# Performance work log

Hardware: AMD Instinct MI355X
Metric: run time of the kernel (lower is better)

The kernel has to match this reference:

```python
import jax, jax.numpy as jnp
import numpy as np

EPS = 1e-5

def layernorm(x, w, b):
    m = jnp.mean(x, axis=-1, keepdims=True)
    v = jnp.var(x, axis=-1, keepdims=True)
    return (x - m) * jax.lax.rsqrt(v + EPS) * w + b

def setup_inputs() -> dict:
    key = jax.random.key(0)
    ks = jax.random.split(key, 20)
    B, N, D, H, C = 4, 2048, 512, 8, 3
    HID = int(D * 4.0 * (2.0 / 3.0))  # SwiGLU hidden = 1365
    g = lambda k, shape, s: (jax.random.normal(k, shape, jnp.float32) * s)
    return {
        "x": g(ks[0], (B, N, D), 1.0),
        "coords": jax.random.uniform(ks[1], (B, N, C), jnp.float32),
        "ln1_w": jnp.ones((D,), jnp.float32),
        "ln1_b": jnp.zeros((D,), jnp.float32),
        "ln2_w": jnp.ones((D,), jnp.float32),
        "ln2_b": jnp.zeros((D,), jnp.float32),
        "Wqkv": g(ks[2], (D, 3 * D), D ** -0.5),
        "bqkv": jnp.zeros((3 * D,), jnp.float32),
        "Wo": g(ks[3], (D, D), D ** -0.5),
        "bo": jnp.zeros((D,), jnp.float32),
        "Wc": g(ks[4], (C, H), 0.1),
        "bc": jnp.zeros((H,), jnp.float32),
        "W1": g(ks[5], (D, HID), D ** -0.5),
        "b1": jnp.zeros((HID,), jnp.float32),
        "W2": g(ks[6], (D, HID), D ** -0.5),
        "b2": jnp.zeros((HID,), jnp.float32),
        "W3": g(ks[7], (HID, D), HID ** -0.5),
        "b3": jnp.zeros((D,), jnp.float32),
    }

def reference(x, coords, ln1_w, ln1_b, ln2_w, ln2_b, Wqkv, bqkv, Wo, bo,
              Wc, bc, W1, b1, W2, b2, W3, b3):
    B, N, D = x.shape
    H = bc.shape[0]
    dh = D // H
    # --- coord-aware patch attention (pre-norm) ---
    h = layernorm(x, ln1_w, ln1_b)
    qkv = h @ Wqkv + bqkv                                # [B,N,3D]
    q, k, v = jnp.split(qkv, 3, axis=-1)
    to_heads = lambda t: t.reshape(B, N, H, dh).transpose(0, 2, 1, 3)  # [B,H,N,dh]
    q, k, v = to_heads(q), to_heads(k), to_heads(v)
    scores = jnp.einsum("bhnd,bhmd->bhnm", q, k) / np.sqrt(dh)
    rel = coords[:, :, None, :] - coords[:, None, :, :]  # [B,N,N,C]
    bias = jnp.einsum("bnmc,ch->bhnm", rel, Wc) + bc[None, :, None, None]
    attn = jax.nn.softmax(scores + bias, axis=-1)
    o = jnp.einsum("bhnm,bhmd->bhnd", attn, v)
    o = o.transpose(0, 2, 1, 3).reshape(B, N, D)
    x = x + (o @ Wo + bo)                                # residual 1
    # --- SwiGLU FFN (pre-norm) ---
    h2 = layernorm(x, ln2_w, ln2_b)
    ff = jax.nn.silu(h2 @ W1 + b1) * (h2 @ W2 + b2)
    x = x + (ff @ W3 + b3)                               # residual 2
    return x
```

## Files before the change

### kernel.cpp

```cpp
#include <hip/hip_runtime.h>
#include <hip/hip_bf16.h>
#include <math.h>

#define B_   4
#define N_   2048
#define D_   512
#define H_   8
#define DH_  64
#define C_   3
#define HID_ 1365
#define HIDP 1408
#define ROWS_ (B_*N_)
#define TD_  (3*D_)

typedef __attribute__((ext_vector_type(8))) short short8;
typedef __attribute__((ext_vector_type(4))) float floatx4;

#define MFMA16(a,b,c) __builtin_amdgcn_mfma_f32_16x16x32_bf16(a,b,c,0,0,0)

typedef __attribute__((address_space(3))) unsigned lds_u32;
typedef __attribute__((address_space(1))) unsigned glb_u32;

__device__ __forceinline__ short sh(float v){
  union { __hip_bfloat16 b; short s; } u;
  u.b = __float2bfloat16(v);
  return u.s;
}

__device__ __forceinline__ int swz(int col, int row){
  return (col & ~63) | (col & 7) | ((((col >> 3) & 7) ^ (row & 7)) << 3);
}

template<int ROWS, int PITCH>
__device__ __forceinline__ void stageG(short* __restrict__ lds,
    const short* __restrict__ g, int ldg, int t){
  const int LPR = PITCH/8;
  const int RPI = 64/LPR;
  const int PW  = (ROWS/RPI)/4;
  int lane = t & 63, w = t >> 6;
  #pragma unroll
  for (int i = 0; i < PW; ++i){
    int r0  = (w*PW + i)*RPI;
    int row = r0 + lane/LPR;
    const short* ga = g + (size_t)row*ldg + (lane % LPR)*8;
    short* la = lds + r0*PITCH;
    __builtin_amdgcn_global_load_lds((const glb_u32*)ga, (lds_u32*)la, 16, 0, 0);
  }
}

__device__ __forceinline__ short8 fragS(const short* __restrict__ lds, int pitch,
    int mbase, int lane, int kk){
  int row  = mbase + (lane & 15);
  int seg  = (kk >> 3) + (lane >> 4);
  int phys = seg ^ (row & 7);
  return *(const short8*)(lds + row*pitch + phys*8);
}

__device__ __forceinline__ short8 fragP(const short* __restrict__ lds,
    int mbase, int lane, int kk){
  return *(const short8*)(lds + (mbase + (lane & 15))*136 + kk + ((lane >> 4) << 3));
}

__global__ __launch_bounds__(256) void convT_all(
    const float* __restrict__ Wqkv, const float* __restrict__ Wo,
    const float* __restrict__ W1, const float* __restrict__ W2,
    const float* __restrict__ W3,
    short* __restrict__ Wtqkv, short* __restrict__ Wto,
    short* __restrict__ Wt1, short* __restrict__ Wt2, short* __restrict__ Wt3,
    const float* __restrict__ coords, const float* __restrict__ Wc,
    float* __restrict__ tv,
    const float* __restrict__ x, const float* __restrict__ ln1_w,
    const float* __restrict__ ln1_b, short* __restrict__ h){
  int id = blockIdx.x;
  int t = threadIdx.x;
  if (id >= 3392){
    int row = id - 3392;
    size_t base = (size_t)row * D_;
    float v0 = x[base + t];
    float v1 = x[base + t + 256];
    float s  = v0 + v1;
    float s2 = v0*v0 + v1*v1;
    #pragma unroll
    for (int off = 32; off >= 1; off >>= 1){
      s  += __shfl_xor(s,  off, 64);
      s2 += __shfl_xor(s2, off, 64);
    }
    __shared__ float red[8];
    int lane = t & 63, wv = t >> 6;
    if (lane == 0){ red[wv] = s; red[4+wv] = s2; }
    __syncthreads();
    float sum  = red[0]+red[1]+red[2]+red[3];
    float sum2 = red[4]+red[5]+red[6]+red[7];
    float mean = sum * (1.0f/D_);
    float var  = sum2 * (1.0f/D_) - mean*mean;
    float inv  = rsqrtf(fmaxf(var, 0.f) + 1e-5f);
    h[base + swz(t,     row)] = sh((v0-mean)*inv*ln1_w[t]     + ln1_b[t]);
    h[base + swz(t+256, row)] = sh((v1-mean)*inv*ln1_w[t+256] + ln1_b[t+256]);
    return;
  }
  if (id >= 3136){
    int idx = (id - 3136)*256 + t;
    int n = idx & (N_-1);
    int hh = (idx >> 11) & (H_-1);
    int b = idx >> 14;
    float s = 0.f;
    #pragma unroll
    for (int cc = 0; cc < C_; ++cc)
      s += coords[((size_t)(b*N_+n))*C_ + cc] * Wc[cc*H_ + hh];
    tv[idx] = s;
    return;
  }
  __shared__ float tile[32][33];
  const float* in; short* out; int K, NN, Kp, nx;
  if (id < 768)      { in=Wqkv; out=Wtqkv; K=512;  NN=1536; Kp=512;  nx=48; }
  else if (id < 1024){ in=Wo;   out=Wto;   K=512;  NN=512;  Kp=512;  nx=16; id-=768; }
  else if (id < 1728){ in=W1;   out=Wt1;   K=512;  NN=HID_; Kp=512;  nx=44; id-=1024; }
  else if (id < 2432){ in=W2;   out=Wt2;   K=512;  NN=HID_; Kp=512;  nx=44; id-=1728; }
  else               { in=W3;   out=Wt3;   K=HID_; NN=512;  Kp=HIDP; nx=16; id-=2432; }
  int nt0 = (id % nx)*32, kt0 = (id / nx)*32;
  int r = t >> 5, cc = t & 31;
  #pragma unroll
  for (int i=0;i<4;++i){
    int k = kt0 + i*8 + r, n = nt0 + cc;
    tile[i*8+r][cc] = (k<K && n<NN) ? in[(size_t)k*NN + n] : 0.f;
  }
  __syncthreads();
  #pragma unroll
  for (int i=0;i<4;++i){
    int n = nt0 + i*8 + r, k = kt0 + cc;
    out[(size_t)n*Kp + swz(k, n)] = sh(tile[cc][i*8+r]);
  }
}

__global__ __launch_bounds__(256) void ln_kernel(const float* __restrict__ x,
        const float* __restrict__ w, const float* __restrict__ b,
        short* __restrict__ out){
  int row = blockIdx.x;
  size_t base = (size_t)row * D_;
  int t = threadIdx.x;
  float v0 = x[base + t];
  float v1 = x[base + t + 256];
  float s  = v0 + v1;
  float s2 = v0*v0 + v1*v1;
  #pragma unroll
  for (int off = 32; off >= 1; off >>= 1){
    s  += __shfl_xor(s,  off, 64);
    s2 += __shfl_xor(s2, off, 64);
  }
  __shared__ float red[8];
  int lane = t & 63, wv = t >> 6;
  if (lane == 0){ red[wv] = s; red[4+wv] = s2; }
  __syncthreads();
  float sum  = red[0]+red[1]+red[2]+red[3];
  float sum2 = red[4]+red[5]+red[6]+red[7];
  float mean = sum * (1.0f/D_);
  float var  = sum2 * (1.0f/D_) - mean*mean;
  float inv  = rsqrtf(fmaxf(var, 0.f) + 1e-5f);
  out[base + swz(t,     row)] = sh((v0-mean)*inv*w[t]     + b[t]);
  out[base + swz(t+256, row)] = sh((v1-mean)*inv*w[t+256] + b[t+256]);
}

__global__ __launch_bounds__(256) void qkv_gemm(
    const short* __restrict__ A, const short* __restrict__ Bt,
    const float* __restrict__ bias,
    short* __restrict__ qb, short* __restrict__ kb, short* __restrict__ vbt){
  __shared__ short As[128*64];
  __shared__ short Bs[128*64];
  int t = threadIdx.x;
  int lane = t & 63, w = t >> 6;
  int wr = (w >> 1) * 64, wc = (w & 1) * 64;
  int col0 = blockIdx.x * 128, row0 = blockIdx.y * 128;
  floatx4 acc[4][4];
  #pragma unroll
  for (int mt=0;mt<4;++mt)
    #pragma unroll
    for (int nt=0;nt<4;++nt) acc[mt][nt] = (floatx4){0.f,0.f,0.f,0.f};
  for (int k0 = 0; k0 < D_; k0 += 64){
    __syncthreads();
    stageG<128,64>(As, A  + (size_t)row0*D_ + k0, D_, t);
    stageG<128,64>(Bs, Bt + (size_t)col0*D_ + k0, D_, t);
    __syncthreads();
    #pragma unroll
    for (int kk = 0; kk < 64; kk += 32){
      short8 af[4], bf[4];
      #pragma unroll
      for (int mt=0;mt<4;++mt) af[mt] = fragS(As, 64, wr+mt*16, lane, kk);
      #pragma unroll
      for (int nt=0;nt<4;++nt) bf[nt] = fragS(Bs, 64, wc+nt*16, lane, kk);
      #pragma unroll
      for (int mt=0;mt<4;++mt)
        #pragma unroll
        for (int nt=0;nt<4;++nt)
          acc[mt][nt] = MFMA16(af[mt], bf[nt], acc[mt][nt]);
    }
  }
  int quad = lane >> 4, c = lane & 15;
  #pragma unroll
  for (int mt=0;mt<4;++mt){
    #pragma unroll
    for (int nt=0;nt<4;++nt){
      #pragma unroll
      for (int r=0;r<4;++r){
        int row = row0 + wr + mt*16 + quad*4 + r;
        int col = col0 + wc + nt*16 + c;
        float v = acc[mt][nt][r] + bias[col];
        int bidx = row >> 11, n = row & (N_-1);
        int which = col >> 9, d = col & (D_-1), hh = d >> 6, hd = d & 63;
        short sv = sh(v);
        if (which == 0)
          qb[(((size_t)(bidx*H_ + hh))*N_ + n)*DH_ + swz(hd, n)] = sv;
        else if (which == 1)
          kb[(((size_t)(bidx*H_ + hh))*N_ + n)*DH_ + swz(hd, n)] = sv;
        else
          vbt[(((size_t)(bidx*H_ + hh))*DH_ + hd)*N_ + swz(n, hd)] = sv;
      }
    }
  }
}

__global__ __launch_bounds__(256) void gemm64(
    const short* __restrict__ A, int lda,
    const short* __restrict__ Bt, int Ktot,
    const float* __restrict__ bias,
    const float* __restrict__ resid, float* __restrict__ outF){
  __shared__ short As[128*64];
  __shared__ short Bs[64*64];
  int t = threadIdx.x, lane = t & 63, w = t >> 6;
  int wr = w * 32;
  int col0 = blockIdx.x * 64, row0 = blockIdx.y * 128;
  floatx4 acc[2][4];
  #pragma unroll
  for (int mt=0;mt<2;++mt)
    #pragma unroll
    for (int nt=0;nt<4;++nt) acc[mt][nt] = (floatx4){0.f,0.f,0.f,0.f};
  for (int k0 = 0; k0 < Ktot; k0 += 64){
    __syncthreads();
    stageG<128,64>(As, A  + (size_t)row0*lda + k0, lda, t);
    stageG<64,64> (Bs, Bt + (size_t)col0*Ktot + k0, Ktot, t);
    __syncthreads();
    #pragma unroll
    for (int kk = 0; kk < 64; kk += 32){
      short8 af[2], bf[4];
      #pragma unroll
      for (int mt=0;mt<2;++mt) af[mt] = fragS(As, 64, wr+mt*16, lane, kk);
      #pragma unroll
      for (int nt=0;nt<4;++nt) bf[nt] = fragS(Bs, 64, nt*16, lane, kk);
      #pragma unroll
      for (int mt=0;mt<2;++mt)
        #pragma unroll
        for (int nt=0;nt<4;++nt)
          acc[mt][nt] = MFMA16(af[mt], bf[nt], acc[mt][nt]);
    }
  }
  int quad = lane >> 4, c = lane & 15;
  #pragma unroll
  for (int mt=0;mt<2;++mt){
    #pragma unroll
    for (int nt=0;nt<4;++nt){
      #pragma unroll
      for (int r=0;r<4;++r){
        int row = row0 + wr + mt*16 + quad*4 + r;
        int col = col0 + nt*16 + c;
        size_t idx = (size_t)row*D_ + col;
        outF[idx] = acc[mt][nt][r] + bias[col] + resid[idx];
      }
    }
  }
}

__global__ __launch_bounds__(256) void gate_gemm(
    const short* __restrict__ A,
    const short* __restrict__ Bt1, const short* __restrict__ Bt2,
    const float* __restrict__ b1, const float* __restrict__ b2,
    short* __restrict__ ff){
  __shared__ short As[128*64];
  __shared__ short B1s[64*64];
  __shared__ short B2s[64*64];
  int t = threadIdx.x, lane = t & 63, w = t >> 6;
  int wr = (w >> 1) * 64, wc = (w & 1) * 32;
  int col0 = blockIdx.x * 64, row0 = blockIdx.y * 128;
  floatx4 a1[4][2], a2[4][2];
  #pragma unroll
  for (int mt=0;mt<4;++mt)
    #pragma unroll
    for (int nt=0;nt<2;++nt){
      a1[mt][nt] = (floatx4){0.f,0.f,0.f,0.f};
      a2[mt][nt] = (floatx4){0.f,0.f,0.f,0.f};
    }
  for (int k0 = 0; k0 < D_; k0 += 64){
    __syncthreads();
    stageG<128,64>(As, A + (size_t)row0*D_ + k0, D_, t);
    stageG<64,64>(B1s, Bt1 + (size_t)col0*D_ + k0, D_, t);
    stageG<64,64>(B2s, Bt2 + (size_t)col0*D_ + k0, D_, t);
    __syncthreads();
    #pragma unroll
    for (int kk = 0; kk < 64; kk += 32){
      short8 af[4], f1[2], f2[2];
      #pragma unroll
      for (int mt=0;mt<4;++mt) af[mt] = fragS(As, 64, wr+mt*16, lane, kk);
      #pragma unroll
      for (int nt=0;nt<2;++nt){
        f1[nt] = fragS(B1s, 64, wc+nt*16, lane, kk);
        f2[nt] = fragS(B2s, 64, wc+nt*16, lane, kk);
      }
      #pragma unroll
      for (int mt=0;mt<4;++mt)
        #pragma unroll
        for (int nt=0;nt<2;++nt){
          a1[mt][nt] = MFMA16(af[mt], f1[nt], a1[mt][nt]);
          a2[mt][nt] = MFMA16(af[mt], f2[nt], a2[mt][nt]);
        }
    }
  }
  int quad = lane >> 4, c = lane & 15;
  #pragma unroll
  for (int mt=0;mt<4;++mt){
    #pragma unroll
    for (int nt=0;nt<2;++nt){
      #pragma unroll
      for (int r=0;r<4;++r){
        int row = row0 + wr + mt*16 + quad*4 + r;
        int col = col0 + wc + nt*16 + c;
        float g1 = a1[mt][nt][r] + (col < HID_ ? b1[col] : 0.f);
        float g2 = a2[mt][nt][r] + (col < HID_ ? b2[col] : 0.f);
        float sig = 1.f / (1.f + __expf(-g1));
        ff[(size_t)row*HIDP + swz(col, row)] = sh(g1*sig*g2);
      }
    }
  }
}

__global__ __launch_bounds__(256) void attn_mfma(
    const short* __restrict__ qb, const short* __restrict__ kb,
    const short* __restrict__ vbt, const float* __restrict__ tv,
    short* __restrict__ o){
  __shared__ short Ks[128*64];
  __shared__ short Vt[64*128];
  __shared__ short Ps[128*136];
  __shared__ float tsh[128];
  int qt = blockIdx.x, h = blockIdx.y, b = blockIdx.z;
  int bh = b*H_ + h;
  int t = threadIdx.x, lane = t & 63, w = t >> 6;
  int quad = lane >> 4, c = lane & 15;
  stageG<128,64>(Ps, qb + ((size_t)bh*N_ + qt*128)*DH_, DH_, t);
  __syncthreads();
  short8 qf[2][2];
  #pragma unroll
  for (int mt=0;mt<2;++mt)
    #pragma unroll
    for (int kh=0;kh<2;++kh)
      qf[mt][kh] = fragS(Ps, 64, w*32 + mt*16, lane, kh*32);

  floatx4 O[2][4];
  float l_i[2][4];
  #pragma unroll
  for (int mt=0;mt<2;++mt){
    #pragma unroll
    for (int nt=0;nt<4;++nt) O[mt][nt] = (floatx4){0.f,0.f,0.f,0.f};
    #pragma unroll
    for (int r=0;r<4;++r) l_i[mt][r] = 0.f;
  }
  const short* Kbase = kb  + (size_t)bh*N_*DH_;
  const short* Vbase = vbt + (size_t)bh*DH_*N_;

  for (int kt = 0; kt < N_/128; ++kt){
    __syncthreads();
    stageG<128,64>(Ks, Kbase + (size_t)kt*128*DH_, DH_, t);
    stageG<64,128>(Vt, Vbase + kt*128, N_, t);
    if (t < 128) tsh[t] = tv[(size_t)bh*N_ + kt*128 + t];
    __syncthreads();

    floatx4 S[2][8];
    #pragma unroll
    for (int mt=0;mt<2;++mt)
      #pragma unroll
      for (int nt=0;nt<8;++nt) S[mt][nt] = (floatx4){0.f,0.f,0.f,0.f};
    #pragma unroll
    for (int kh=0;kh<2;++kh){
      short8 kf[8];
      #pragma unroll
      for (int nt=0;nt<8;++nt) kf[nt] = fragS(Ks, 64, nt*16, lane, kh*32);
      #pragma unroll
      for (int mt=0;mt<2;++mt)
        #pragma unroll
        for (int nt=0;nt<8;++nt)
          S[mt][nt] = MFMA16(qf[mt][kh], kf[nt], S[mt][nt]);
    }
    float ts[8];
    #pragma unroll
    for (int nt=0;nt<8;++nt) ts[nt] = tsh[nt*16 + c];
    #pragma unroll
    for (int mt=0;mt<2;++mt)
      #pragma unroll
      for (int r=0;r<4;++r){
        #pragma unroll
        for (int nt=0;nt<8;++nt){
          float p = __expf(S[mt][nt][r]*0.125f - ts[nt]);
          l_i[mt][r] += p;
          Ps[(w*32 + mt*16 + quad*4 + r)*136 + nt*16 + c] = sh(p);
        }
      }
    asm volatile("s_waitcnt lgkmcnt(0)" ::: "memory");
    #pragma unroll
    for (int kh=0;kh<4;++kh){
      short8 vf[4], pf[2];
      #pragma unroll
      for (int nt=0;nt<4;++nt) vf[nt] = fragS(Vt, 128, nt*16, lane, kh*32);
      #pragma unroll
      for (int mt=0;mt<2;++mt) pf[mt] = fragP(Ps, w*32 + mt*16, lane, kh*32);
      #pragma unroll
      for (int mt=0;mt<2;++mt)
        #pragma unroll
        for (int nt=0;nt<4;++nt)
          O[mt][nt] = MFMA16(pf[mt], vf[nt], O[mt][nt]);
    }
  }
  #pragma unroll
  for (int mt=0;mt<2;++mt){
    #pragma unroll
    for (int r=0;r<4;++r){
      float l = l_i[mt][r];
      #pragma unroll
      for (int off=1; off<16; off<<=1) l += __shfl_xor(l, off, 64);
      float invl = 1.f / l;
      int row = qt*128 + w*32 + mt*16 + quad*4 + r;
      #pragma unroll
      for (int nt=0;nt<4;++nt){
        int col = h*DH_ + nt*16 + c;
        o[((size_t)(b*N_ + row))*D_ + swz(col, row)] = sh(O[mt][nt][r]*invl);
      }
    }
  }
}

extern "C" void kernel_launch(void* const* d_in, const int* in_sizes, int n_in,
                              void* d_out, int out_size, void* d_ws, size_t ws_size,
                              hipStream_t stream){
  const float* x      = (const float*)d_in[0];
  const float* coords = (const float*)d_in[1];
  const float* ln1_w  = (const float*)d_in[2];
  const float* ln1_b  = (const float*)d_in[3];
  const float* ln2_w  = (const float*)d_in[4];
  const float* ln2_b  = (const float*)d_in[5];
  const float* Wqkv   = (const float*)d_in[6];
  const float* bqkv   = (const float*)d_in[7];
  const float* Wo     = (const float*)d_in[8];
  const float* bo     = (const float*)d_in[9];
  const float* Wc     = (const float*)d_in[10];
  const float* W1     = (const float*)d_in[12];
  const float* b1     = (const float*)d_in[13];
  const float* W2     = (const float*)d_in[14];
  const float* b2     = (const float*)d_in[15];
  const float* W3     = (const float*)d_in[16];
  const float* b3     = (const float*)d_in[17];

  char* ws = (char*)d_ws;
  short* Wtqkv = (short*)(ws);
  short* Wto   = (short*)(ws + 1572864);
  short* Wt1   = (short*)(ws + 2097152);
  short* Wt2   = (short*)(ws + 3538944);
  short* Wt3   = (short*)(ws + 4980736);
  float* tv    = (float*)(ws + 6422528);
  short* h     = (short*)(ws + 6684672);
  short* qb    = (short*)(ws + 15073280);
  short* kb    = (short*)(ws + 23461888);
  short* vbt   = (short*)(ws + 31850496);
  short* o     = h;
  short* h2    = h;
  short* ff    = qb;
  float* x1    = (float*)d_out;

  convT_all<<<dim3(11584), dim3(256), 0, stream>>>(Wqkv, Wo, W1, W2, W3,
      Wtqkv, Wto, Wt1, Wt2, Wt3, coords, Wc, tv, x, ln1_w, ln1_b, h);
  qkv_gemm<<<dim3(12,64), dim3(256), 0, stream>>>(h, Wtqkv, bqkv, qb, kb, vbt);
  attn_mfma<<<dim3(16,8,4), dim3(256), 0, stream>>>(qb, kb, vbt, tv, o);
  gemm64<<<dim3(8,64), dim3(256), 0, stream>>>(o, 512, Wto, 512, bo, x, x1);
  ln_kernel<<<dim3(ROWS_), dim3(256), 0, stream>>>(x1, ln2_w, ln2_b, h2);
  gate_gemm<<<dim3(22,64), dim3(256), 0, stream>>>(h2, Wt1, Wt2, b1, b2, ff);
  gemm64<<<dim3(8,64), dim3(256), 0, stream>>>(ff, HIDP, Wt3, HIDP, b3, x1, x1);
}
```

Baseline: 313.1 us.

## Double-buffer K/V in attention and keep P in registers via permlane swaps

Rewrites the attention kernel to double-buffer K and V tiles in LDS so the next tile loads while the current one computes, with one barrier per iteration instead of two. It computes S transposed (K as the A operand) so the probabilities can be packed into bf16 and rearranged with permlane32/16 swaps straight into PV MFMA operands, dropping the LDS round-trip for P. It also preloads the whole per-head bias term once, switches to exp2 with a folded scale, and writes the output as packed vector stores. The cost is more LDS for the double buffers and the full bias array, which may reduce occupancy.

```diff
diff --git a/kernel.cpp b/kernel.cpp
--- a/kernel.cpp
+++ b/kernel.cpp
@@ -15,6 +15,7 @@
 
 typedef __attribute__((ext_vector_type(8))) short short8;
 typedef __attribute__((ext_vector_type(4))) float floatx4;
+typedef __attribute__((ext_vector_type(2))) unsigned uint2v;
 
 #define MFMA16(a,b,c) __builtin_amdgcn_mfma_f32_16x16x32_bf16(a,b,c,0,0,0)
 
@@ -25,6 +26,12 @@
   union { __hip_bfloat16 b; short s; } u;
   u.b = __float2bfloat16(v);
   return u.s;
+}
+
+__device__ __forceinline__ unsigned pk2(float a, float b){
+  union { short s[2]; unsigned u; } z;
+  z.s[0] = sh(a); z.s[1] = sh(b);
+  return z.u;
 }
 
 __device__ __forceinline__ int swz(int col, int row){
@@ -54,11 +61,6 @@
   int seg  = (kk >> 3) + (lane >> 4);
   int phys = seg ^ (row & 7);
   return *(const short8*)(lds + row*pitch + phys*8);
-}
-
-__device__ __forceinline__ short8 fragP(const short* __restrict__ lds,
-    int mbase, int lane, int kk){
-  return *(const short8*)(lds + (mbase + (lane & 15))*136 + kk + ((lane >> 4) << 3));
 }
 
 __global__ __launch_bounds__(256) void convT_all(
@@ -330,105 +332,116 @@
   }
 }
 
+#define EXP2SC 0.18033688011112042f
 __global__ __launch_bounds__(256) void attn_mfma(
-    const short* __restrict__ qb, const short* __restrict__ kb,
+    const short* __restrict__ qb, const short* __restrict__ kbuf,
     const short* __restrict__ vbt, const float* __restrict__ tv,
     short* __restrict__ o){
-  __shared__ short Ks[128*64];
-  __shared__ short Vt[64*128];
-  __shared__ short Ps[128*136];
-  __shared__ float tsh[128];
+  __shared__ short Ks2[2][128*64];
+  __shared__ short Vt2[2][64*128];
+  __shared__ __align__(16) float tsAll[2048];
   int qt = blockIdx.x, h = blockIdx.y, b = blockIdx.z;
   int bh = b*H_ + h;
   int t = threadIdx.x, lane = t & 63, w = t >> 6;
   int quad = lane >> 4, c = lane & 15;
-  stageG<128,64>(Ps, qb + ((size_t)bh*N_ + qt*128)*DH_, DH_, t);
+  const short* Kbase = kbuf + (size_t)bh*N_*DH_;
+  const short* Vbase = vbt  + (size_t)bh*DH_*N_;
+
+  #pragma unroll
+  for (int i = 0; i < 8; ++i)
+    tsAll[i*256 + t] = tv[(size_t)bh*N_ + i*256 + t] * 1.44269504f;
+  stageG<128,64>(Ks2[1], qb + ((size_t)bh*N_ + qt*128)*DH_, DH_, t);
+  stageG<128,64>(Ks2[0], Kbase, DH_, t);
+  stageG<64,128>(Vt2[0], Vbase, N_, t);
   __syncthreads();
   short8 qf[2][2];
   #pragma unroll
   for (int mt=0;mt<2;++mt)
     #pragma unroll
     for (int kh=0;kh<2;++kh)
-      qf[mt][kh] = fragS(Ps, 64, w*32 + mt*16, lane, kh*32);
-
+      qf[mt][kh] = fragS(Ks2[1], 64, w*32 + mt*16, lane, kh*32);
   floatx4 O[2][4];
-  float l_i[2][4];
+  float l_i[2] = {0.f, 0.f};
+  #pragma unroll
+  for (int mt=0;mt<2;++mt)
+    #pragma unroll
+    for (int nt=0;nt<4;++nt) O[mt][nt] = (floatx4){0.f,0.f,0.f,0.f};
+  __syncthreads();
+
+  for (int kt = 0; kt < N_/128; ++kt){
+    int cur = kt & 1;
+    if (kt + 1 < N_/128){
+      stageG<128,64>(Ks2[cur^1], Kbase + (size_t)(kt+1)*128*DH_, DH_, t);
+      stageG<64,128>(Vt2[cur^1], Vbase + (kt+1)*128, N_, t);
+    }
+    const short* Kc  = Ks2[cur];
+    const short* Vc  = Vt2[cur];
+    const float* tsc = tsAll + kt*128;
+    #pragma unroll
+    for (int kb4 = 0; kb4 < 4; ++kb4){
+      floatx4 St[2][2];
+      #pragma unroll
+      for (int i=0;i<2;++i){
+        St[i][0] = (floatx4){0.f,0.f,0.f,0.f};
+        St[i][1] = (floatx4){0.f,0.f,0.f,0.f};
+      }
+      #pragma unroll
+      for (int kh=0;kh<2;++kh){
+        short8 kf0 = fragS(Kc, 64, kb4*32,      lane, kh*32);
+        short8 kf1 = fragS(Kc, 64, kb4*32 + 16, lane, kh*32);
+        #pragma unroll
+        for (int mt=0;mt<2;++mt){
+          St[0][mt] = MFMA16(kf0, qf[mt][kh], St[0][mt]);
+          St[1][mt] = MFMA16(kf1, qf[mt][kh], St[1][mt]);
+        }
+      }
+      floatx4 t0 = *(const floatx4*)&tsc[kb4*32 + quad*4];
+      floatx4 t1 = *(const floatx4*)&tsc[kb4*32 + 16 + quad*4];
+      short8 pbf[2];
+      #pragma unroll
+      for (int mt=0;mt<2;++mt){
+        float p0[4], p1[4];
+        #pragma unroll
+        for (int r=0;r<4;++r){
+          p0[r] = __builtin_amdgcn_exp2f(fmaf(St[0][mt][r], EXP2SC, -t0[r]));
+          p1[r] = __builtin_amdgcn_exp2f(fmaf(St[1][mt][r], EXP2SC, -t1[r]));
+        }
+        l_i[mt] += (p0[0]+p0[1]) + (p0[2]+p0[3]) + (p1[0]+p1[1]) + (p1[2]+p1[3]);
+        unsigned X0 = pk2(p0[0], p0[1]), X1 = pk2(p0[2], p0[3]);
+        unsigned Y0 = pk2(p1[0], p1[1]), Y1 = pk2(p1[2], p1[3]);
+        auto u0 = __builtin_amdgcn_permlane32_swap(X0, Y0, false, false);
+        auto v0 = __builtin_amdgcn_permlane16_swap(u0[0], u0[1], false, false);
+        auto u1 = __builtin_amdgcn_permlane32_swap(X1, Y1, false, false);
+        auto v1 = __builtin_amdgcn_permlane16_swap(u1[0], u1[1], false, false);
+        union { short8 s; unsigned uu[4]; } pb;
+        pb.uu[0] = v0[0]; pb.uu[1] = v1[0]; pb.uu[2] = v0[1]; pb.uu[3] = v1[1];
+        pbf[mt] = pb.s;
+      }
+      #pragma unroll
+      for (int nt=0;nt<4;++nt){
+        short8 vf = fragS(Vc, 128, nt*16, lane, kb4*32);
+        #pragma unroll
+        for (int mt=0;mt<2;++mt)
+          O[mt][nt] = MFMA16(vf, pbf[mt], O[mt][nt]);
+      }
+    }
+    __syncthreads();
+  }
   #pragma unroll
   for (int mt=0;mt<2;++mt){
-    #pragma unroll
-    for (int nt=0;nt<4;++nt) O[mt][nt] = (floatx4){0.f,0.f,0.f,0.f};
-    #pragma unroll
-    for (int r=0;r<4;++r) l_i[mt][r] = 0.f;
-  }
-  const short* Kbase = kb  + (size_t)bh*N_*DH_;
-  const short* Vbase = vbt + (size_t)bh*DH_*N_;
-
-  for (int kt = 0; kt < N_/128; ++kt){
-    __syncthreads();
-    stageG<128,64>(Ks, Kbase + (size_t)kt*128*DH_, DH_, t);
-    stageG<64,128>(Vt, Vbase + kt*128, N_, t);
-    if (t < 128) tsh[t] = tv[(size_t)bh*N_ + kt*128 + t];
-    __syncthreads();
-
-    floatx4 S[2][8];
-    #pragma unroll
-    for (int mt=0;mt<2;++mt)
-      #pragma unroll
-      for (int nt=0;nt<8;++nt) S[mt][nt] = (floatx4){0.f,0.f,0.f,0.f};
-    #pragma unroll
-    for (int kh=0;kh<2;++kh){
-      short8 kf[8];
-      #pragma unroll
-      for (int nt=0;nt<8;++nt) kf[nt] = fragS(Ks, 64, nt*16, lane, kh*32);
-      #pragma unroll
-      for (int mt=0;mt<2;++mt)
-        #pragma unroll
-        for (int nt=0;nt<8;++nt)
-          S[mt][nt] = MFMA16(qf[mt][kh], kf[nt], S[mt][nt]);
-    }
-    float ts[8];
-    #pragma unroll
-    for (int nt=0;nt<8;++nt) ts[nt] = tsh[nt*16 + c];
-    #pragma unroll
-    for (int mt=0;mt<2;++mt)
-      #pragma unroll
-      for (int r=0;r<4;++r){
-        #pragma unroll
-        for (int nt=0;nt<8;++nt){
-          float p = __expf(S[mt][nt][r]*0.125f - ts[nt]);
-          l_i[mt][r] += p;
-          Ps[(w*32 + mt*16 + quad*4 + r)*136 + nt*16 + c] = sh(p);
-        }
-      }
-    asm volatile("s_waitcnt lgkmcnt(0)" ::: "memory");
-    #pragma unroll
-    for (int kh=0;kh<4;++kh){
-      short8 vf[4], pf[2];
-      #pragma unroll
-      for (int nt=0;nt<4;++nt) vf[nt] = fragS(Vt, 128, nt*16, lane, kh*32);
-      #pragma unroll
-      for (int mt=0;mt<2;++mt) pf[mt] = fragP(Ps, w*32 + mt*16, lane, kh*32);
-      #pragma unroll
-      for (int mt=0;mt<2;++mt)
-        #pragma unroll
-        for (int nt=0;nt<4;++nt)
-          O[mt][nt] = MFMA16(pf[mt], vf[nt], O[mt][nt]);
-    }
-  }
-  #pragma unroll
-  for (int mt=0;mt<2;++mt){
-    #pragma unroll
-    for (int r=0;r<4;++r){
-      float l = l_i[mt][r];
-      #pragma unroll
-      for (int off=1; off<16; off<<=1) l += __shfl_xor(l, off, 64);
-      float invl = 1.f / l;
-      int row = qt*128 + w*32 + mt*16 + quad*4 + r;
-      #pragma unroll
-      for (int nt=0;nt<4;++nt){
-        int col = h*DH_ + nt*16 + c;
-        o[((size_t)(b*N_ + row))*D_ + swz(col, row)] = sh(O[mt][nt][r]*invl);
-      }
+    float l = l_i[mt];
+    l += __shfl_xor(l, 16, 64);
+    l += __shfl_xor(l, 32, 64);
+    float invl = 1.f / l;
+    int qrow = qt*128 + w*32 + mt*16 + c;
+    size_t rb = ((size_t)b*N_ + qrow)*(size_t)D_;
+    #pragma unroll
+    for (int nt=0;nt<4;++nt){
+      int d0 = h*DH_ + nt*16 + quad*4;
+      uint2v pv;
+      pv.x = pk2(O[mt][nt][0]*invl, O[mt][nt][1]*invl);
+      pv.y = pk2(O[mt][nt][2]*invl, O[mt][nt][3]*invl);
+      *(uint2v*)(o + rb + swz(d0, qrow)) = pv;
     }
   }
 }
```

Measured after the change: 310.8 us. No clear change (-0.7%).
